# Kernel optimization log

Hardware: AMD Instinct MI355X
Metric: run time of the kernel (lower is better)

## Reference

```python
import jax, jax.numpy as jnp
import numpy as np

N, E, G = 50000, 400000, 2000
H, HEADS, HD = 128, 4, 32


def setup_inputs() -> dict:
    key = jax.random.key(0)
    ks = jax.random.split(key, 16)
    nrm = lambda k, shape, s=0.05: jax.random.normal(k, shape, dtype=jnp.float32) * s
    inp = {}
    inp["x"] = jax.random.normal(ks[0], (N, 39), dtype=jnp.float32)
    inp["edge_index"] = jax.random.randint(ks[1], (2, E), 0, N, dtype=jnp.int32)
    inp["edge_attr"] = jax.random.normal(ks[2], (E, 8), dtype=jnp.float32)
    inp["batch"] = jnp.sort(jax.random.randint(ks[3], (N,), 0, G, dtype=jnp.int32))
    inp["in_W"] = nrm(ks[4], (39, H)); inp["in_b"] = jnp.zeros((H,), jnp.float32)
    inp["in_g"] = jnp.ones((H,), jnp.float32); inp["in_beta"] = jnp.zeros((H,), jnp.float32)
    inp["Wl"] = nrm(ks[5], (3, H, H)); inp["Wr"] = nrm(ks[6], (3, H, H))
    inp["We"] = nrm(ks[7], (3, 8, H)); inp["att"] = nrm(ks[8], (3, HEADS, HD))
    inp["conv_b"] = jnp.zeros((3, H), jnp.float32)
    inp["bn_g"] = jnp.ones((3, H), jnp.float32); inp["bn_b"] = jnp.zeros((3, H), jnp.float32)
    inp["t1_W"] = nrm(ks[9], (3 * H, 256)); inp["t1_b"] = jnp.zeros((256,), jnp.float32)
    inp["t1_g"] = jnp.ones((256,), jnp.float32); inp["t1_beta"] = jnp.zeros((256,), jnp.float32)
    inp["t2_W"] = nrm(ks[10], (256, 128)); inp["t2_b"] = jnp.zeros((128,), jnp.float32)
    inp["t2_g"] = jnp.ones((128,), jnp.float32); inp["t2_beta"] = jnp.zeros((128,), jnp.float32)
    inp["head_W"] = nrm(ks[11], (128, 12)); inp["head_b"] = jnp.zeros((12,), jnp.float32)
    return inp


def _bn(h, g, b):
    # BatchNorm1d in training mode: normalize with batch statistics.
    m = h.mean(0)
    v = ((h - m) ** 2).mean(0)
    return g * (h - m) * jax.lax.rsqrt(v + 1e-5) + b


def reference(x, edge_index, edge_attr, batch, in_W, in_b, in_g, in_beta,
              Wl, Wr, We, att, conv_b, bn_g, bn_b,
              t1_W, t1_b, t1_g, t1_beta, t2_W, t2_b, t2_g, t2_beta,
              head_W, head_b):
    src, dst = edge_index[0], edge_index[1]  # messages flow src -> dst (PyG convention)
    xn = jax.nn.relu(_bn(x @ in_W + in_b, in_g, in_beta))  # [N, H]
    for l in range(3):  # three residual GATv2 layers
        xl = (xn @ Wl[l]).reshape(N, HEADS, HD)  # lin_l (source transform)
        xr = (xn @ Wr[l]).reshape(N, HEADS, HD)  # lin_r (target transform)
        ep = (edge_attr @ We[l]).reshape(E, HEADS, HD)
        m = jax.nn.leaky_relu(xl[src] + xr[dst] + ep, 0.2)  # [E, HEADS, HD]
        alpha = jnp.einsum('ehd,hd->eh', m, att[l])  # [E, HEADS]
        amax = jax.ops.segment_max(alpha, dst, num_segments=N)
        amax = jnp.where(jnp.isfinite(amax), amax, 0.0)  # nodes with no in-edges
        ae = jnp.exp(alpha - amax[dst])
        denom = jax.ops.segment_sum(ae, dst, num_segments=N)
        a = ae / (denom[dst] + 1e-16)  # scatter-softmax over neighborhoods
        agg = jax.ops.segment_sum(xl[src] * a[:, :, None], dst, num_segments=N)
        h = agg.reshape(N, H) + conv_b[l]
        h = jax.nn.elu(_bn(h, bn_g[l], bn_b[l]))
        xn = xn + h
    # 3-way global pooling per graph
    cnt = jax.ops.segment_sum(jnp.ones((N,), jnp.float32), batch, num_segments=G)
    sadd = jax.ops.segment_sum(xn, batch, num_segments=G)
    smean = sadd / jnp.maximum(cnt, 1.0)[:, None]
    smax = jax.ops.segment_max(xn, batch, num_segments=G)
    smax = jnp.where(cnt[:, None] > 0, smax, 0.0)
    xg = jnp.concatenate([smean, smax, sadd], axis=1)  # [G, 3H]
    t = jax.nn.relu(_bn(xg @ t1_W + t1_b, t1_g, t1_beta))
    t = jax.nn.relu(_bn(t @ t2_W + t2_b, t2_g, t2_beta))
    return jax.nn.sigmoid(t @ head_W + head_b)  # [G, 12]
```

## Files before the change

### kernel.cpp

```cpp
#include <hip/hip_runtime.h>
#include <math.h>


constexpr int N_ = 50000;
constexpr int E_ = 400000;
constexpr int G_ = 2000;
constexpr int H_ = 128;
constexpr int IN_ = 39;
constexpr int NT_ = (N_ + 63) / 64;

typedef __attribute__((ext_vector_type(8))) short bf16x8;
typedef __attribute__((ext_vector_type(4))) float f32x4;

__device__ __forceinline__ unsigned pk_bf16(float a, float b) {
  unsigned ua = __float_as_uint(a);
  unsigned ub = __float_as_uint(b);
  ua = (ua + 0x7fffu + ((ua >> 16) & 1u)) >> 16;
  ub = (ub + 0x7fffu + ((ub >> 16) & 1u)) & 0xffff0000u;
  return ua | ub;
}
__device__ __forceinline__ unsigned short bf16_1(float x) {
  unsigned u = __float_as_uint(x);
  u = (u + 0x7fffu + ((u >> 16) & 1u)) >> 16;
  return (unsigned short)u;
}
__device__ __forceinline__ float up_lo(unsigned u) { return __uint_as_float(u << 16); }
__device__ __forceinline__ float up_hi(unsigned u) { return __uint_as_float(u & 0xffff0000u); }

__global__ __launch_bounds__(256) void hist_kernel(const int* __restrict__ keys, int n,
                                                   int* __restrict__ cnt) {
  for (int i = blockIdx.x * 256 + threadIdx.x; i < n; i += gridDim.x * 256)
    atomicAdd(&cnt[keys[i]], 1);
}

__global__ __launch_bounds__(1024) void scan_local(const int* __restrict__ in,
                                                   int* __restrict__ outx,
                                                   int* __restrict__ bsum, int n) {
  __shared__ int wsum[16];
  int t = threadIdx.x, lane = t & 63, wid = t >> 6;
  int idx = blockIdx.x * 1024 + t;
  int v = (idx < n) ? in[idx] : 0;
  int x = v;
#pragma unroll
  for (int off = 1; off < 64; off <<= 1) {
    int y = __shfl_up(x, off, 64);
    if (lane >= off) x += y;
  }
  if (lane == 63) wsum[wid] = x;
  __syncthreads();
  if (t == 0) {
    int acc = 0;
#pragma unroll
    for (int w = 0; w < 16; w++) { int tmp = wsum[w]; wsum[w] = acc; acc += tmp; }
    bsum[blockIdx.x] = acc;
  }
  __syncthreads();
  if (idx < n) outx[idx] = wsum[wid] + x - v;
}

__global__ __launch_bounds__(64) void scan_bsum(const int* __restrict__ bsum,
                                                int* __restrict__ boff, int nb) {
  int t = threadIdx.x;
  int v = (t < nb) ? bsum[t] : 0;
  int x = v;
#pragma unroll
  for (int off = 1; off < 64; off <<= 1) {
    int y = __shfl_up(x, off, 64);
    if (t >= off) x += y;
  }
  boff[t] = x - v;
}

__global__ __launch_bounds__(1024) void scan_add(int* __restrict__ eoff,
                                                 const int* __restrict__ boff,
                                                 int* __restrict__ cursor, int n) {
  int idx = blockIdx.x * 1024 + threadIdx.x;
  if (idx < n) {
    int e = eoff[idx] + boff[idx >> 10];
    eoff[idx] = e;
    cursor[idx] = e;
  }
  if (idx == 0) eoff[n] = E_;
}

__global__ __launch_bounds__(256) void goff_from_sorted(const int* __restrict__ batch,
                                                        int* __restrict__ goff) {
  int i = blockIdx.x * 256 + threadIdx.x;
  if (i >= N_) return;
  int bi = batch[i];
  int bp = (i == 0) ? -1 : batch[i - 1];
  for (int g = bp + 1; g <= bi; g++) goff[g] = i;
  if (i == N_ - 1) {
    for (int g = bi + 1; g <= G_; g++) goff[g] = N_;
  }
}

__global__ __launch_bounds__(256) void edge_scatter(const int* __restrict__ ei,
                                                    const float* __restrict__ ea,
                                                    int* __restrict__ cursor,
                                                    int* __restrict__ esrc,
                                                    unsigned* __restrict__ easb) {
  int e = blockIdx.x * 256 + threadIdx.x;
  if (e >= E_) return;
  int src = ei[e];
  int dst = ei[E_ + e];
  int j = atomicAdd(&cursor[dst], 1);
  esrc[j] = src;
  const float4* eav = (const float4*)(ea + (size_t)e * 8);
  float4 a0 = eav[0], a1 = eav[1];
  uint4 o;
  o.x = pk_bf16(a0.x, a0.y);
  o.y = pk_bf16(a0.z, a0.w);
  o.z = pk_bf16(a1.x, a1.y);
  o.w = pk_bf16(a1.z, a1.w);
  ((uint4*)easb)[j] = o;
}

__global__ __launch_bounds__(256) void pack_weights(const float* __restrict__ Wl,
                                                    const float* __restrict__ Wr,
                                                    unsigned short* __restrict__ wpack) {
  int i = blockIdx.x * 256 + threadIdx.x;
  if (i >= 3 * 128 * 256) return;
  int l = i >> 15;
  int rem = i & 32767;
  int k = rem >> 8;
  int n = rem & 255;
  const float* Wsrc = (n < 128) ? (Wl + l * H_ * H_) : (Wr + l * H_ * H_);
  int nn = n & 127;
  wpack[(size_t)l * 32768 + n * 128 + k] = bf16_1(Wsrc[k * H_ + nn]);
}

__global__ __launch_bounds__(256) void in_gemm(const float* __restrict__ x,
                                               const float* __restrict__ W,
                                               const float* __restrict__ b,
                                               float* __restrict__ y,
                                               float* __restrict__ ssum,
                                               float* __restrict__ ssq) {
  __shared__ float xs[32][40];
  __shared__ float s1[256], s2[256];
  int t = threadIdx.x;
  int row0 = blockIdx.x * 32;
  for (int i = t; i < 32 * IN_; i += 256) {
    int r = i / IN_, k = i % IN_;
    int row = row0 + r;
    xs[r][k] = (row < N_) ? x[row * IN_ + k] : 0.f;
  }
  __syncthreads();
  int col = t & 127;
  int half = t >> 7;
  float acc[16];
#pragma unroll
  for (int r = 0; r < 16; r++) acc[r] = 0.f;
  for (int k = 0; k < IN_; k++) {
    float w = W[k * H_ + col];
#pragma unroll
    for (int r = 0; r < 16; r++) acc[r] = fmaf(xs[half * 16 + r][k], w, acc[r]);
  }
  float bb = b[col];
  float a1 = 0.f, a2 = 0.f;
#pragma unroll
  for (int r = 0; r < 16; r++) {
    int row = row0 + half * 16 + r;
    float v = acc[r] + bb;
    if (row < N_) {
      y[row * H_ + col] = v;
      a1 += v;
      a2 = fmaf(v, v, a2);
    }
  }
  s1[t] = a1; s2[t] = a2;
  __syncthreads();
  if (t < 128) {
    atomicAdd(&ssum[t], s1[t] + s1[t + 128]);
    atomicAdd(&ssq[t], s2[t] + s2[t + 128]);
  }
}

template <int MODE>
__global__ __launch_bounds__(256) void gemm_mfma(const float* __restrict__ xn_in,
                                                 float* __restrict__ xn_out,
                                                 const float* __restrict__ buf,
                                                 const float* __restrict__ g,
                                                 const float* __restrict__ beta,
                                                 const float* __restrict__ ssum,
                                                 const float* __restrict__ ssq,
                                                 float rows_inv,
                                                 const unsigned short* __restrict__ wp,
                                                 unsigned* __restrict__ xlb,
                                                 unsigned* __restrict__ xrb) {
  __shared__ short a_s[64][136];
  __shared__ short b_s[128][136];
  int t = threadIdx.x;
  int lane = t & 63, w = t >> 6;
  int quad = lane >> 4, lc = lane & 15;
  int type = blockIdx.x & 1;
  unsigned* xout = type ? xrb : xlb;

  {
    const unsigned short* wbase = wp + (size_t)type * 16384;
    int nl = t >> 1;
    int kh = (t & 1) * 64;
#pragma unroll
    for (int v4 = 0; v4 < 8; v4++)
      *(uint4*)&b_s[nl][kh + v4 * 8] = *(const uint4*)&wbase[nl * 128 + kh + v4 * 8];
  }

  int stride = gridDim.x >> 1;
  for (int tile = blockIdx.x >> 1; tile < NT_; tile += stride) {
    int row0 = tile * 64;
    __syncthreads();
    {
      int r = t >> 2;
      int row = row0 + r;
      int kb0 = (t & 3) * 32;
      bool valid = row < N_;
      for (int kk = 0; kk < 32; kk += 4) {
        int c = kb0 + kk;
        float4 v = make_float4(0.f, 0.f, 0.f, 0.f);
        if (valid) {
          float4 bv = *(const float4*)&buf[(size_t)row * H_ + c];
          float4 gv = *(const float4*)&g[c];
          float4 be = *(const float4*)&beta[c];
          float4 s1 = *(const float4*)&ssum[c];
          float4 s2 = *(const float4*)&ssq[c];
          float m0 = s1.x * rows_inv, m1 = s1.y * rows_inv;
          float m2 = s1.z * rows_inv, m3 = s1.w * rows_inv;
          float r0 = rsqrtf(s2.x * rows_inv - m0 * m0 + 1e-5f);
          float r1 = rsqrtf(s2.y * rows_inv - m1 * m1 + 1e-5f);
          float r2 = rsqrtf(s2.z * rows_inv - m2 * m2 + 1e-5f);
          float r3 = rsqrtf(s2.w * rows_inv - m3 * m3 + 1e-5f);
          float t0 = gv.x * (bv.x - m0) * r0 + be.x;
          float t1 = gv.y * (bv.y - m1) * r1 + be.y;
          float t2 = gv.z * (bv.z - m2) * r2 + be.z;
          float t3 = gv.w * (bv.w - m3) * r3 + be.w;
          if (MODE == 1) {
            v = make_float4(fmaxf(t0, 0.f), fmaxf(t1, 0.f), fmaxf(t2, 0.f), fmaxf(t3, 0.f));
          } else {
            float4 xo = *(const float4*)&xn_in[(size_t)row * H_ + c];
            v.x = xo.x + ((t0 > 0.f) ? t0 : (__expf(t0) - 1.f));
            v.y = xo.y + ((t1 > 0.f) ? t1 : (__expf(t1) - 1.f));
            v.z = xo.z + ((t2 > 0.f) ? t2 : (__expf(t2) - 1.f));
            v.w = xo.w + ((t3 > 0.f) ? t3 : (__expf(t3) - 1.f));
          }
          if (type == 0) *(float4*)&xn_out[(size_t)row * H_ + c] = v;
        }
        uint2 pk;
        pk.x = pk_bf16(v.x, v.y);
        pk.y = pk_bf16(v.z, v.w);
        *(uint2*)&a_s[r][c] = pk;
      }
    }
    __syncthreads();

    f32x4 acc[8];
#pragma unroll
    for (int nt = 0; nt < 8; nt++) acc[nt] = (f32x4){0.f, 0.f, 0.f, 0.f};
#pragma unroll
    for (int kb = 0; kb < 4; kb++) {
      bf16x8 av = *(const bf16x8*)&a_s[w * 16 + lc][kb * 32 + quad * 8];
#pragma unroll
      for (int nt = 0; nt < 8; nt++) {
        bf16x8 bv = *(const bf16x8*)&b_s[nt * 16 + lc][kb * 32 + quad * 8];
        acc[nt] = __builtin_amdgcn_mfma_f32_16x16x32_bf16(av, bv, acc[nt], 0, 0, 0);
      }
    }

    int rowg0 = row0 + w * 16 + quad * 4;
#pragma unroll
    for (int nt = 0; nt < 8; nt++) {
#pragma unroll
      for (int rr = 0; rr < 4; rr++) {
        float v = acc[nt][rr];
        float pv = __shfl_xor(v, 1, 64);
        int rowg = rowg0 + rr;
        if (!(lc & 1) && rowg < N_) {
          unsigned u = pk_bf16(v, pv);
          xout[(size_t)rowg * 64 + nt * 8 + (lc >> 1)] = u;
        }
      }
    }
  }
}

__device__ __forceinline__ float ep8u(const uint4& u, const float* w) {
  float ep = up_lo(u.x) * w[0];
  ep = fmaf(up_hi(u.x), w[1], ep);
  ep = fmaf(up_lo(u.y), w[2], ep);
  ep = fmaf(up_hi(u.y), w[3], ep);
  ep = fmaf(up_lo(u.z), w[4], ep);
  ep = fmaf(up_hi(u.z), w[5], ep);
  ep = fmaf(up_lo(u.w), w[6], ep);
  ep = fmaf(up_hi(u.w), w[7], ep);
  return ep;
}

__global__ __launch_bounds__(256) void agg_csr(const int* __restrict__ eoff,
                                               const int* __restrict__ esrc,
                                               const unsigned* __restrict__ easb,
                                               const float* __restrict__ Wel,
                                               const float* __restrict__ attl,
                                               const unsigned* __restrict__ xlb,
                                               const unsigned* __restrict__ xrb,
                                               const float* __restrict__ cb,
                                               float* __restrict__ buf,
                                               float* __restrict__ ssum,
                                               float* __restrict__ ssq) {
  __shared__ float sA[256], sB[256], sC[256], sD[256];
  int t = threadIdx.x;
  int l = t & 63;
  int sub = t >> 6;
  int c0 = l * 2;
  float w0[8], w1[8];
#pragma unroll
  for (int k = 0; k < 8; k++) {
    float2 wv = *(const float2*)&Wel[k * H_ + c0];
    w0[k] = wv.x; w1[k] = wv.y;
  }
  float2 attv = *(const float2*)&attl[c0];
  float2 cbv = *(const float2*)&cb[c0];
  const uint4* eas4 = (const uint4*)easb;
  float a1_0 = 0.f, a1_1 = 0.f, a2_0 = 0.f, a2_1 = 0.f;
  for (int n = blockIdx.x * 4 + sub; n < N_; n += gridDim.x * 4) {
    unsigned xru = xrb[(size_t)n * 64 + l];
    float xr0 = up_lo(xru), xr1 = up_hi(xru);
    int e0 = eoff[n], e1 = eoff[n + 1];
    float acc0 = 0.f, acc1 = 0.f, den = 0.f;
    int j = e0;
    for (; j + 4 <= e1; j += 4) {
      int s0 = esrc[j], s1 = esrc[j + 1], s2 = esrc[j + 2], s3 = esrc[j + 3];
      uint4 u0 = eas4[j], u1 = eas4[j + 1], u2 = eas4[j + 2], u3 = eas4[j + 3];
      unsigned xu0 = xlb[(size_t)s0 * 64 + l];
      unsigned xu1 = xlb[(size_t)s1 * 64 + l];
      unsigned xu2 = xlb[(size_t)s2 * 64 + l];
      unsigned xu3 = xlb[(size_t)s3 * 64 + l];
      float x00 = up_lo(xu0), x01 = up_hi(xu0);
      float x10 = up_lo(xu1), x11 = up_hi(xu1);
      float x20 = up_lo(xu2), x21 = up_hi(xu2);
      float x30 = up_lo(xu3), x31 = up_hi(xu3);
      float m00 = x00 + xr0 + ep8u(u0, w0);
      float m01 = x01 + xr1 + ep8u(u0, w1);
      float m10 = x10 + xr0 + ep8u(u1, w0);
      float m11 = x11 + xr1 + ep8u(u1, w1);
      float m20 = x20 + xr0 + ep8u(u2, w0);
      float m21 = x21 + xr1 + ep8u(u2, w1);
      float m30 = x30 + xr0 + ep8u(u3, w0);
      float m31 = x31 + xr1 + ep8u(u3, w1);
      m00 = (m00 > 0.f) ? m00 : 0.2f * m00;
      m01 = (m01 > 0.f) ? m01 : 0.2f * m01;
      m10 = (m10 > 0.f) ? m10 : 0.2f * m10;
      m11 = (m11 > 0.f) ? m11 : 0.2f * m11;
      m20 = (m20 > 0.f) ? m20 : 0.2f * m20;
      m21 = (m21 > 0.f) ? m21 : 0.2f * m21;
      m30 = (m30 > 0.f) ? m30 : 0.2f * m30;
      m31 = (m31 > 0.f) ? m31 : 0.2f * m31;
      float p0 = fmaf(m00, attv.x, m01 * attv.y);
      float p1 = fmaf(m10, attv.x, m11 * attv.y);
      float p2 = fmaf(m20, attv.x, m21 * attv.y);
      float p3 = fmaf(m30, attv.x, m31 * attv.y);
#pragma unroll
      for (int off = 8; off > 0; off >>= 1) {
        p0 += __shfl_xor(p0, off, 64);
        p1 += __shfl_xor(p1, off, 64);
        p2 += __shfl_xor(p2, off, 64);
        p3 += __shfl_xor(p3, off, 64);
      }
      float e0v = __expf(p0), e1v = __expf(p1), e2v = __expf(p2), e3v = __expf(p3);
      acc0 = fmaf(e0v, x00, acc0); acc1 = fmaf(e0v, x01, acc1);
      acc0 = fmaf(e1v, x10, acc0); acc1 = fmaf(e1v, x11, acc1);
      acc0 = fmaf(e2v, x20, acc0); acc1 = fmaf(e2v, x21, acc1);
      acc0 = fmaf(e3v, x30, acc0); acc1 = fmaf(e3v, x31, acc1);
      den += (e0v + e1v) + (e2v + e3v);
    }
    for (; j < e1; j++) {
      int s0 = esrc[j];
      uint4 u0 = eas4[j];
      unsigned xu0 = xlb[(size_t)s0 * 64 + l];
      float x00 = up_lo(xu0), x01 = up_hi(xu0);
      float m00 = x00 + xr0 + ep8u(u0, w0);
      float m01 = x01 + xr1 + ep8u(u0, w1);
      m00 = (m00 > 0.f) ? m00 : 0.2f * m00;
      m01 = (m01 > 0.f) ? m01 : 0.2f * m01;
      float p0 = fmaf(m00, attv.x, m01 * attv.y);
#pragma unroll
      for (int off = 8; off > 0; off >>= 1) p0 += __shfl_xor(p0, off, 64);
      float e0v = __expf(p0);
      acc0 = fmaf(e0v, x00, acc0);
      acc1 = fmaf(e0v, x01, acc1);
      den += e0v;
    }
    float inv = 1.f / (den + 1e-16f);
    float h0 = acc0 * inv + cbv.x;
    float h1 = acc1 * inv + cbv.y;
    *(float2*)&buf[(size_t)n * H_ + c0] = make_float2(h0, h1);
    a1_0 += h0; a1_1 += h1;
    a2_0 = fmaf(h0, h0, a2_0); a2_1 = fmaf(h1, h1, a2_1);
  }
  sA[t] = a1_0; sB[t] = a1_1; sC[t] = a2_0; sD[t] = a2_1;
  __syncthreads();
  if (t < 64) {
    float r1 = sA[t] + sA[t + 64] + sA[t + 128] + sA[t + 192];
    float r2 = sB[t] + sB[t + 64] + sB[t + 128] + sB[t + 192];
    float r3 = sC[t] + sC[t + 64] + sC[t + 128] + sC[t + 192];
    float r4 = sD[t] + sD[t + 64] + sD[t + 128] + sD[t + 192];
    atomicAdd(&ssum[2 * t], r1);
    atomicAdd(&ssum[2 * t + 1], r2);
    atomicAdd(&ssq[2 * t], r3);
    atomicAdd(&ssq[2 * t + 1], r4);
  }
}

__global__ __launch_bounds__(256) void apply_bn_relu(const float* __restrict__ y,
                                                     float* __restrict__ out,
                                                     const float* __restrict__ g,
                                                     const float* __restrict__ beta,
                                                     const float* __restrict__ ssum,
                                                     const float* __restrict__ ssq,
                                                     float rows_inv,
                                                     long total, int cmask) {
  long i = (long)blockIdx.x * 256 + threadIdx.x;
  if (i >= total) return;
  int c = (int)i & cmask;
  float m = ssum[c] * rows_inv;
  float rs = rsqrtf(ssq[c] * rows_inv - m * m + 1e-5f);
  float v = g[c] * (y[i] - m) * rs + beta[c];
  out[i] = fmaxf(v, 0.f);
}

__global__ __launch_bounds__(128) void pool_residual(const int* __restrict__ goff,
                                                     const float* __restrict__ xn,
                                                     const float* __restrict__ buf,
                                                     const float* __restrict__ g,
                                                     const float* __restrict__ beta,
                                                     const float* __restrict__ ssum,
                                                     const float* __restrict__ ssq,
                                                     float rows_inv,
                                                     float* __restrict__ xg) {
  int gr = blockIdx.x;
  int t = threadIdx.x;
  int n0 = goff[gr], n1 = goff[gr + 1];
  float mm = ssum[t] * rows_inv;
  float rr = rsqrtf(ssq[t] * rows_inv - mm * mm + 1e-5f);
  float gg = g[t], bb = beta[t];
  float s = 0.f, mx = -INFINITY;
  for (int n = n0; n < n1; n++) {
    float w = gg * (buf[(size_t)n * H_ + t] - mm) * rr + bb;
    w = (w > 0.f) ? w : (__expf(w) - 1.f);
    float v = xn[(size_t)n * H_ + t] + w;
    s += v;
    mx = fmaxf(mx, v);
  }
  float c = (float)(n1 - n0);
  xg[gr * 384 + t] = s / fmaxf(c, 1.f);
  xg[gr * 384 + 128 + t] = (c > 0.f) ? mx : 0.f;
  xg[gr * 384 + 256 + t] = s;
}

template <int K, int COLS>
__global__ void mlp_gemm(const float* __restrict__ A, const float* __restrict__ W,
                         const float* __restrict__ b, float* __restrict__ Y, int rows,
                         float* __restrict__ ssum, float* __restrict__ ssq) {
  __shared__ float xs[8][K];
  int t = threadIdx.x;
  int row0 = blockIdx.x * 8;
  for (int i = t; i < 8 * K; i += COLS) {
    int r = i / K, k = i % K;
    int row = row0 + r;
    xs[r][k] = (row < rows) ? A[row * K + k] : 0.f;
  }
  __syncthreads();
  float acc[8];
#pragma unroll
  for (int r = 0; r < 8; r++) acc[r] = 0.f;
  for (int k = 0; k < K; k++) {
    float w = W[k * COLS + t];
#pragma unroll
    for (int r = 0; r < 8; r++) acc[r] = fmaf(xs[r][k], w, acc[r]);
  }
  float bb = b[t];
  float a1 = 0.f, a2 = 0.f;
#pragma unroll
  for (int r = 0; r < 8; r++) {
    int row = row0 + r;
    if (row < rows) {
      float v = acc[r] + bb;
      Y[row * COLS + t] = v;
      a1 += v;
      a2 = fmaf(v, v, a2);
    }
  }
  atomicAdd(&ssum[t], a1);
  atomicAdd(&ssq[t], a2);
}

__global__ __launch_bounds__(64) void head_kernel(const float* __restrict__ u,
                                                  const float* __restrict__ W,
                                                  const float* __restrict__ b,
                                                  float* __restrict__ out) {
  __shared__ float row[128];
  int g = blockIdx.x;
  int t = threadIdx.x;
  row[t] = u[g * 128 + t];
  row[t + 64] = u[g * 128 + 64 + t];
  __syncthreads();
  if (t < 12) {
    float acc = b[t];
    for (int k = 0; k < 128; k++) acc = fmaf(row[k], W[k * 12 + t], acc);
    out[g * 12 + t] = 1.f / (1.f + expf(-acc));
  }
}

extern "C" void kernel_launch(void* const* d_in, const int* in_sizes, int n_in, void* d_out,
                              int out_size, void* d_ws, size_t ws_size, hipStream_t stream) {
  (void)in_sizes; (void)n_in; (void)out_size; (void)ws_size;
  const float* x       = (const float*)d_in[0];
  const int*   ei      = (const int*)d_in[1];
  const float* ea      = (const float*)d_in[2];
  const int*   batch   = (const int*)d_in[3];
  const float* in_W    = (const float*)d_in[4];
  const float* in_b    = (const float*)d_in[5];
  const float* in_g    = (const float*)d_in[6];
  const float* in_beta = (const float*)d_in[7];
  const float* Wl      = (const float*)d_in[8];
  const float* Wr      = (const float*)d_in[9];
  const float* We      = (const float*)d_in[10];
  const float* att     = (const float*)d_in[11];
  const float* conv_b  = (const float*)d_in[12];
  const float* bn_g    = (const float*)d_in[13];
  const float* bn_b    = (const float*)d_in[14];
  const float* t1_W    = (const float*)d_in[15];
  const float* t1_b    = (const float*)d_in[16];
  const float* t1_g    = (const float*)d_in[17];
  const float* t1_beta = (const float*)d_in[18];
  const float* t2_W    = (const float*)d_in[19];
  const float* t2_b    = (const float*)d_in[20];
  const float* t2_g    = (const float*)d_in[21];
  const float* t2_beta = (const float*)d_in[22];
  const float* head_W  = (const float*)d_in[23];
  const float* head_b  = (const float*)d_in[24];
  float* out = (float*)d_out;

  float* p = (float*)d_ws;
  float* xnA   = p; p += N_ * H_;
  float* xnB   = p; p += N_ * H_;
  float* buf   = p; p += N_ * H_;
  float* sstat = p; p += 6 * 512;
  float* xg    = p; p += G_ * 384;
  float* u1    = p; p += G_ * 256;
  float* u2    = p; p += G_ * 128;
  unsigned* up = (unsigned*)p;
  unsigned* xlb  = up; up += (size_t)N_ * 64;
  unsigned* xrb  = up; up += (size_t)N_ * 64;
  unsigned* easb = up; up += (size_t)E_ * 4;
  unsigned short* wpack = (unsigned short*)up; up += 3 * 32768 / 2;
  int* ip = (int*)up;
  int* deg    = ip; ip += N_;
  int* eoff   = ip; ip += N_ + 1;
  int* cursor = ip; ip += N_;
  int* goff   = ip; ip += G_ + 1;
  int* esrc   = ip; ip += E_;
  int* bsum   = ip; ip += 64;
  int* boff   = ip; ip += 64;

#define SSUM(s) (sstat + (s) * 512)
#define SSQ(s)  (sstat + (s) * 512 + 256)

  hipMemsetAsync(deg, 0, (size_t)N_ * sizeof(int), stream);
  hipMemsetAsync(sstat, 0, 6 * 512 * sizeof(float), stream);
  hist_kernel<<<1024, 256, 0, stream>>>(ei + E_, E_, deg);
  scan_local<<<49, 1024, 0, stream>>>(deg, eoff, bsum, N_);
  scan_bsum<<<1, 64, 0, stream>>>(bsum, boff, 49);
  scan_add<<<49, 1024, 0, stream>>>(eoff, boff, cursor, N_);
  edge_scatter<<<(E_ + 255) / 256, 256, 0, stream>>>(ei, ea, cursor, esrc, easb);
  goff_from_sorted<<<(N_ + 255) / 256, 256, 0, stream>>>(batch, goff);
  pack_weights<<<384, 256, 0, stream>>>(Wl, Wr, wpack);

  in_gemm<<<(N_ + 31) / 32, 256, 0, stream>>>(x, in_W, in_b, buf, SSUM(0), SSQ(0));

  const float rnInv = 1.f / N_;
  gemm_mfma<1><<<768, 256, 0, stream>>>(xnA, xnA, buf, in_g, in_beta, SSUM(0), SSQ(0), rnInv,
                                        wpack, xlb, xrb);
  agg_csr<<<2048, 256, 0, stream>>>(eoff, esrc, easb, We, att, xlb, xrb, conv_b,
                                    buf, SSUM(1), SSQ(1));
  gemm_mfma<2><<<768, 256, 0, stream>>>(xnA, xnB, buf, bn_g, bn_b, SSUM(1), SSQ(1), rnInv,
                                        wpack + 32768, xlb, xrb);
  agg_csr<<<2048, 256, 0, stream>>>(eoff, esrc, easb, We + 8 * H_, att + H_, xlb, xrb,
                                    conv_b + H_, buf, SSUM(2), SSQ(2));
  gemm_mfma<2><<<768, 256, 0, stream>>>(xnB, xnA, buf, bn_g + H_, bn_b + H_, SSUM(2), SSQ(2),
                                        rnInv, wpack + 65536, xlb, xrb);
  agg_csr<<<2048, 256, 0, stream>>>(eoff, esrc, easb, We + 16 * H_, att + 2 * H_, xlb, xrb,
                                    conv_b + 2 * H_, buf, SSUM(3), SSQ(3));

  pool_residual<<<G_, 128, 0, stream>>>(goff, xnA, buf, bn_g + 2 * H_, bn_b + 2 * H_,
                                        SSUM(3), SSQ(3), rnInv, xg);

  const float rgInv = 1.f / G_;
  mlp_gemm<384, 256><<<G_ / 8, 256, 0, stream>>>(xg, t1_W, t1_b, u1, G_, SSUM(4), SSQ(4));
  apply_bn_relu<<<(G_ * 256 + 255) / 256, 256, 0, stream>>>(u1, u1, t1_g, t1_beta,
                                                            SSUM(4), SSQ(4), rgInv,
                                                            (long)G_ * 256, 255);

  mlp_gemm<256, 128><<<G_ / 8, 128, 0, stream>>>(u1, t2_W, t2_b, u2, G_, SSUM(5), SSQ(5));
  apply_bn_relu<<<(G_ * 128 + 255) / 256, 256, 0, stream>>>(u2, u2, t2_g, t2_beta,
                                                            SSUM(5), SSQ(5), rgInv,
                                                            (long)G_ * 128, 127);

  head_kernel<<<G_, 64, 0, stream>>>(u2, head_W, head_b, out);
#undef SSUM
#undef SSQ
}
```

Measured before the change: 946.4 us.

## Compute both Wl and Wr projections per row tile, reading weights from global

The MFMA GEMM now has each block handle one 64-row tile and produce both the lin_l and lin_r outputs (16 N-tiles), instead of a persistent grid where blocks alternated between the two weight matrices. The BN/activation prologue on each input row now runs once rather than twice. The LDS weight staging is dropped and B fragments are read straight from global/L2. The residual is updated in place in a single xn buffer. This removes duplicated prologue work and the per-block weight copy, at the cost of more registers for accumulators and uncached-in-LDS weight reads.

```diff
diff --git a/kernel.cpp b/kernel.cpp
--- a/kernel.cpp
+++ b/kernel.cpp
@@ -7,7 +7,6 @@
 constexpr int G_ = 2000;
 constexpr int H_ = 128;
 constexpr int IN_ = 39;
-constexpr int NT_ = (N_ + 63) / 64;
 
 typedef __attribute__((ext_vector_type(8))) short bf16x8;
 typedef __attribute__((ext_vector_type(4))) float f32x4;
@@ -177,8 +176,7 @@
 }
 
 template <int MODE>
-__global__ __launch_bounds__(256) void gemm_mfma(const float* __restrict__ xn_in,
-                                                 float* __restrict__ xn_out,
+__global__ __launch_bounds__(256) void gemm_mfma(float* __restrict__ xn,
                                                  const float* __restrict__ buf,
                                                  const float* __restrict__ g,
                                                  const float* __restrict__ beta,
@@ -189,94 +187,80 @@
                                                  unsigned* __restrict__ xlb,
                                                  unsigned* __restrict__ xrb) {
   __shared__ short a_s[64][136];
-  __shared__ short b_s[128][136];
   int t = threadIdx.x;
   int lane = t & 63, w = t >> 6;
   int quad = lane >> 4, lc = lane & 15;
-  int type = blockIdx.x & 1;
-  unsigned* xout = type ? xrb : xlb;
+  int row0 = blockIdx.x * 64;
 
   {
-    const unsigned short* wbase = wp + (size_t)type * 16384;
-    int nl = t >> 1;
-    int kh = (t & 1) * 64;
-#pragma unroll
-    for (int v4 = 0; v4 < 8; v4++)
-      *(uint4*)&b_s[nl][kh + v4 * 8] = *(const uint4*)&wbase[nl * 128 + kh + v4 * 8];
-  }
-
-  int stride = gridDim.x >> 1;
-  for (int tile = blockIdx.x >> 1; tile < NT_; tile += stride) {
-    int row0 = tile * 64;
-    __syncthreads();
-    {
-      int r = t >> 2;
-      int row = row0 + r;
-      int kb0 = (t & 3) * 32;
-      bool valid = row < N_;
-      for (int kk = 0; kk < 32; kk += 4) {
-        int c = kb0 + kk;
-        float4 v = make_float4(0.f, 0.f, 0.f, 0.f);
-        if (valid) {
-          float4 bv = *(const float4*)&buf[(size_t)row * H_ + c];
-          float4 gv = *(const float4*)&g[c];
-          float4 be = *(const float4*)&beta[c];
-          float4 s1 = *(const float4*)&ssum[c];
-          float4 s2 = *(const float4*)&ssq[c];
-          float m0 = s1.x * rows_inv, m1 = s1.y * rows_inv;
-          float m2 = s1.z * rows_inv, m3 = s1.w * rows_inv;
-          float r0 = rsqrtf(s2.x * rows_inv - m0 * m0 + 1e-5f);
-          float r1 = rsqrtf(s2.y * rows_inv - m1 * m1 + 1e-5f);
-          float r2 = rsqrtf(s2.z * rows_inv - m2 * m2 + 1e-5f);
-          float r3 = rsqrtf(s2.w * rows_inv - m3 * m3 + 1e-5f);
-          float t0 = gv.x * (bv.x - m0) * r0 + be.x;
-          float t1 = gv.y * (bv.y - m1) * r1 + be.y;
-          float t2 = gv.z * (bv.z - m2) * r2 + be.z;
-          float t3 = gv.w * (bv.w - m3) * r3 + be.w;
-          if (MODE == 1) {
-            v = make_float4(fmaxf(t0, 0.f), fmaxf(t1, 0.f), fmaxf(t2, 0.f), fmaxf(t3, 0.f));
-          } else {
-            float4 xo = *(const float4*)&xn_in[(size_t)row * H_ + c];
-            v.x = xo.x + ((t0 > 0.f) ? t0 : (__expf(t0) - 1.f));
-            v.y = xo.y + ((t1 > 0.f) ? t1 : (__expf(t1) - 1.f));
-            v.z = xo.z + ((t2 > 0.f) ? t2 : (__expf(t2) - 1.f));
-            v.w = xo.w + ((t3 > 0.f) ? t3 : (__expf(t3) - 1.f));
-          }
-          if (type == 0) *(float4*)&xn_out[(size_t)row * H_ + c] = v;
+    int r = t >> 2;
+    int row = row0 + r;
+    int kb0 = (t & 3) * 32;
+    bool valid = row < N_;
+    for (int kk = 0; kk < 32; kk += 4) {
+      int c = kb0 + kk;
+      float4 v = make_float4(0.f, 0.f, 0.f, 0.f);
+      if (valid) {
+        float4 bv = *(const float4*)&buf[(size_t)row * H_ + c];
+        float4 gv = *(const float4*)&g[c];
+        float4 be = *(const float4*)&beta[c];
+        float4 s1 = *(const float4*)&ssum[c];
+        float4 s2 = *(const float4*)&ssq[c];
+        float m0 = s1.x * rows_inv, m1 = s1.y * rows_inv;
+        float m2 = s1.z * rows_inv, m3 = s1.w * rows_inv;
+        float r0 = rsqrtf(s2.x * rows_inv - m0 * m0 + 1e-5f);
+        float r1 = rsqrtf(s2.y * rows_inv - m1 * m1 + 1e-5f);
+        float r2 = rsqrtf(s2.z * rows_inv - m2 * m2 + 1e-5f);
+        float r3 = rsqrtf(s2.w * rows_inv - m3 * m3 + 1e-5f);
+        float t0 = gv.x * (bv.x - m0) * r0 + be.x;
+        float t1 = gv.y * (bv.y - m1) * r1 + be.y;
+        float t2 = gv.z * (bv.z - m2) * r2 + be.z;
+        float t3 = gv.w * (bv.w - m3) * r3 + be.w;
+        if (MODE == 1) {
+          v = make_float4(fmaxf(t0, 0.f), fmaxf(t1, 0.f), fmaxf(t2, 0.f), fmaxf(t3, 0.f));
+        } else {
+          float4 xo = *(const float4*)&xn[(size_t)row * H_ + c];
+          v.x = xo.x + ((t0 > 0.f) ? t0 : (__expf(t0) - 1.f));
+          v.y = xo.y + ((t1 > 0.f) ? t1 : (__expf(t1) - 1.f));
+          v.z = xo.z + ((t2 > 0.f) ? t2 : (__expf(t2) - 1.f));
+          v.w = xo.w + ((t3 > 0.f) ? t3 : (__expf(t3) - 1.f));
         }
-        uint2 pk;
-        pk.x = pk_bf16(v.x, v.y);
-        pk.y = pk_bf16(v.z, v.w);
-        *(uint2*)&a_s[r][c] = pk;
+        *(float4*)&xn[(size_t)row * H_ + c] = v;
       }
-    }
-    __syncthreads();
-
-    f32x4 acc[8];
-#pragma unroll
-    for (int nt = 0; nt < 8; nt++) acc[nt] = (f32x4){0.f, 0.f, 0.f, 0.f};
-#pragma unroll
-    for (int kb = 0; kb < 4; kb++) {
-      bf16x8 av = *(const bf16x8*)&a_s[w * 16 + lc][kb * 32 + quad * 8];
-#pragma unroll
-      for (int nt = 0; nt < 8; nt++) {
-        bf16x8 bv = *(const bf16x8*)&b_s[nt * 16 + lc][kb * 32 + quad * 8];
-        acc[nt] = __builtin_amdgcn_mfma_f32_16x16x32_bf16(av, bv, acc[nt], 0, 0, 0);
-      }
-    }
-
-    int rowg0 = row0 + w * 16 + quad * 4;
-#pragma unroll
-    for (int nt = 0; nt < 8; nt++) {
-#pragma unroll
-      for (int rr = 0; rr < 4; rr++) {
-        float v = acc[nt][rr];
-        float pv = __shfl_xor(v, 1, 64);
-        int rowg = rowg0 + rr;
-        if (!(lc & 1) && rowg < N_) {
-          unsigned u = pk_bf16(v, pv);
-          xout[(size_t)rowg * 64 + nt * 8 + (lc >> 1)] = u;
-        }
+      uint2 pk;
+      pk.x = pk_bf16(v.x, v.y);
+      pk.y = pk_bf16(v.z, v.w);
+      *(uint2*)&a_s[r][c] = pk;
+    }
+  }
+  __syncthreads();
+
+  f32x4 acc[16];
+#pragma unroll
+  for (int nt = 0; nt < 16; nt++) acc[nt] = (f32x4){0.f, 0.f, 0.f, 0.f};
+#pragma unroll
+  for (int kb = 0; kb < 4; kb++) {
+    bf16x8 av = *(const bf16x8*)&a_s[w * 16 + lc][kb * 32 + quad * 8];
+#pragma unroll
+    for (int nt = 0; nt < 16; nt++) {
+      bf16x8 bv = *(const bf16x8*)&wp[(size_t)(nt * 16 + lc) * 128 + kb * 32 + quad * 8];
+      acc[nt] = __builtin_amdgcn_mfma_f32_16x16x32_bf16(av, bv, acc[nt], 0, 0, 0);
+    }
+  }
+
+  int rowg0 = row0 + w * 16 + quad * 4;
+#pragma unroll
+  for (int nt = 0; nt < 16; nt++) {
+    unsigned* xout = (nt < 8) ? xlb : xrb;
+    int cp0 = (nt < 8) ? nt * 8 : (nt - 8) * 8;
+#pragma unroll
+    for (int rr = 0; rr < 4; rr++) {
+      float v = acc[nt][rr];
+      float pv = __shfl_xor(v, 1, 64);
+      int rowg = rowg0 + rr;
+      if (!(lc & 1) && rowg < N_) {
+        unsigned u = pk_bf16(v, pv);
+        xout[(size_t)rowg * 64 + cp0 + (lc >> 1)] = u;
       }
     }
   }
@@ -540,8 +524,7 @@
   float* out = (float*)d_out;
 
   float* p = (float*)d_ws;
-  float* xnA   = p; p += N_ * H_;
-  float* xnB   = p; p += N_ * H_;
+  float* xn    = p; p += N_ * H_;
   float* buf   = p; p += N_ * H_;
   float* sstat = p; p += 6 * 512;
   float* xg    = p; p += G_ * 384;
@@ -577,20 +560,21 @@
   in_gemm<<<(N_ + 31) / 32, 256, 0, stream>>>(x, in_W, in_b, buf, SSUM(0), SSQ(0));
 
   const float rnInv = 1.f / N_;
-  gemm_mfma<1><<<768, 256, 0, stream>>>(xnA, xnA, buf, in_g, in_beta, SSUM(0), SSQ(0), rnInv,
-                                        wpack, xlb, xrb);
+  const int GT = (N_ + 63) / 64;
+  gemm_mfma<1><<<GT, 256, 0, stream>>>(xn, buf, in_g, in_beta, SSUM(0), SSQ(0), rnInv,
+                                       wpack, xlb, xrb);
   agg_csr<<<2048, 256, 0, stream>>>(eoff, esrc, easb, We, att, xlb, xrb, conv_b,
                                     buf, SSUM(1), SSQ(1));
-  gemm_mfma<2><<<768, 256, 0, stream>>>(xnA, xnB, buf, bn_g, bn_b, SSUM(1), SSQ(1), rnInv,
-                                        wpack + 32768, xlb, xrb);
+  gemm_mfma<2><<<GT, 256, 0, stream>>>(xn, buf, bn_g, bn_b, SSUM(1), SSQ(1), rnInv,
+                                       wpack + 32768, xlb, xrb);
   agg_csr<<<2048, 256, 0, stream>>>(eoff, esrc, easb, We + 8 * H_, att + H_, xlb, xrb,
                                     conv_b + H_, buf, SSUM(2), SSQ(2));
-  gemm_mfma<2><<<768, 256, 0, stream>>>(xnB, xnA, buf, bn_g + H_, bn_b + H_, SSUM(2), SSQ(2),
-                                        rnInv, wpack + 65536, xlb, xrb);
+  gemm_mfma<2><<<GT, 256, 0, stream>>>(xn, buf, bn_g + H_, bn_b + H_, SSUM(2), SSQ(2),
+                                       rnInv, wpack + 65536, xlb, xrb);
   agg_csr<<<2048, 256, 0, stream>>>(eoff, esrc, easb, We + 16 * H_, att + 2 * H_, xlb, xrb,
                                     conv_b + 2 * H_, buf, SSUM(3), SSQ(3));
 
-  pool_residual<<<G_, 128, 0, stream>>>(goff, xnA, buf, bn_g + 2 * H_, bn_b + 2 * H_,
+  pool_residual<<<G_, 128, 0, stream>>>(goff, xn, buf, bn_g + 2 * H_, bn_b + 2 * H_,
                                         SSUM(3), SSQ(3), rnInv, xg);
 
   const float rgInv = 1.f / G_;
```

Measured after the change: 919.9 us. 1.03x faster.
